# Kernel optimization log

Hardware: AMD Instinct MI355X
Metric: run time of the kernel (lower is better)

Reference implementation:

```python
import jax, jax.numpy as jnp
import numpy as np

B = 32768
K = 8           # moe_num_experts
LATENT = 256    # latent_dim
COND = 1024     # fusion_hidden_dim
HID = 128       # moe_expert_hidden_dim
EIN = LATENT + COND + 1  # expert input dim = 1281


def setup_inputs() -> dict:
    key = jax.random.key(0)
    ks = jax.random.split(key, 12)
    cond = jax.random.normal(ks[0], (B, COND), dtype=jnp.float32)
    u = jax.random.normal(ks[1], (B, LATENT), dtype=jnp.float32)
    tau = jax.random.uniform(ks[2], (B, 1), dtype=jnp.float32)
    # posterior gate: positive, sums to 1 over K (realistic p_hat)
    p_raw = jax.random.uniform(ks[3], (B, K), dtype=jnp.float32)
    p_hat = p_raw / jnp.sum(p_raw, axis=-1, keepdims=True)
    s = 0.02
    W1 = jax.random.normal(ks[4], (K, EIN, HID), dtype=jnp.float32) * s
    b1 = jnp.zeros((K, HID), dtype=jnp.float32)
    W2 = jax.random.normal(ks[5], (K, HID, HID), dtype=jnp.float32) * s
    b2 = jnp.zeros((K, HID), dtype=jnp.float32)
    W3 = jax.random.normal(ks[6], (K, HID, LATENT), dtype=jnp.float32) * s
    b3 = jnp.zeros((K, LATENT), dtype=jnp.float32)
    return {"cond": cond, "u": u, "tau": tau, "p_hat": p_hat,
            "W1": W1, "b1": b1, "W2": W2, "b2": b2, "W3": W3, "b3": b3}


def reference(cond, u, tau, p_hat, W1, b1, W2, b2, W3, b3):
    # Training path: gate = p_hat (no smooth switching, no running gate).
    x = jnp.concatenate([u, cond, tau], axis=-1)           # (B, EIN)
    h = jax.nn.silu(jnp.einsum('bd,kdh->bkh', x, W1) + b1) # (B, K, HID)
    h = jax.nn.silu(jnp.einsum('bkh,khg->bkg', h, W2) + b2)
    v_experts = jnp.einsum('bkg,kgl->bkl', h, W3) + b3     # (B, K, LATENT)
    v = jnp.einsum('bk,bkl->bl', p_hat, v_experts)         # (B, LATENT)
    return v
```

## Files before the change

kernel.cpp:

```cpp
#include <hip/hip_runtime.h>
#include <stdint.h>

typedef unsigned short u16;
typedef __attribute__((ext_vector_type(8))) short short8;
typedef __attribute__((ext_vector_type(4))) float f32x4;
typedef __attribute__((ext_vector_type(4))) uint32_t u32x4;

#define KEXP   8
#define LATENT 256
#define CONDD  1024
#define HID    128
#define EIN    1281
#define EINP   1344
#define NCH    21
#define NTOT   1024
#define BROWS  32768

__device__ __forceinline__ u16 f2bf(float x) {
  uint32_t v = __float_as_uint(x);
  v += 0x7fffu + ((v >> 16) & 1u);
  return (u16)(v >> 16);
}

__device__ __forceinline__ void async16(const void* g, void* l) {
  __builtin_amdgcn_global_load_lds(
      (const __attribute__((address_space(1))) void*)g,
      (__attribute__((address_space(3))) void*)l, 16, 0, 0);
}

__device__ __forceinline__ float silu(float x) { return x / (1.f + __expf(-x)); }

#define W1_TILES (KEXP * 42 * 4)
#define W2_TILES (KEXP * 4 * 4)
#define W3_TILES (KEXP * 4 * 8)

__global__ void conv_w(const float* __restrict__ W1, const float* __restrict__ W2,
                       const float* __restrict__ W3,
                       u16* __restrict__ W1t, u16* __restrict__ W2t, u16* __restrict__ W3t2) {
  __shared__ float t[32][33];
  const int bid = blockIdx.x;
  const int tx = threadIdx.x & 31, ty = threadIdx.x >> 5;
  if (bid < W1_TILES) {
    int k = bid / 168, r = bid % 168;
    int d0 = (r / 4) * 32, h0 = (r % 4) * 32;
    const float* src = W1 + (size_t)k * EIN * HID;
    #pragma unroll
    for (int s = 0; s < 4; ++s) {
      int d = d0 + ty + s * 8;
      t[ty + s * 8][tx] = (d < EIN) ? src[(size_t)d * HID + h0 + tx] : 0.f;
    }
    __syncthreads();
    u16* dst = W1t + (size_t)k * HID * EINP;
    #pragma unroll
    for (int s = 0; s < 4; ++s)
      dst[(size_t)(h0 + ty + s * 8) * EINP + d0 + tx] = f2bf(t[tx][ty + s * 8]);
  } else if (bid < W1_TILES + W2_TILES) {
    int j = bid - W1_TILES;
    int k = j / 16, r = j % 16;
    int d0 = (r / 4) * 32, h0 = (r % 4) * 32;
    const float* src = W2 + (size_t)k * HID * HID;
    #pragma unroll
    for (int s = 0; s < 4; ++s)
      t[ty + s * 8][tx] = src[(size_t)(d0 + ty + s * 8) * HID + h0 + tx];
    __syncthreads();
    u16* dst = W2t + (size_t)k * HID * HID;
    #pragma unroll
    for (int s = 0; s < 4; ++s)
      dst[(size_t)(h0 + ty + s * 8) * HID + d0 + tx] = f2bf(t[tx][ty + s * 8]);
  } else {
    int j = bid - W1_TILES - W2_TILES;
    int k = j / 32, r = j % 32;
    int d0 = (r / 8) * 32, h0 = (r % 8) * 32;
    const float* src = W3 + (size_t)k * HID * LATENT;
    #pragma unroll
    for (int s = 0; s < 4; ++s)
      t[ty + s * 8][tx] = src[(size_t)(d0 + ty + s * 8) * LATENT + h0 + tx];
    __syncthreads();
    #pragma unroll
    for (int s = 0; s < 4; ++s)
      W3t2[(size_t)(h0 + ty + s * 8) * NTOT + k * HID + d0 + tx] = f2bf(t[tx][ty + s * 8]);
  }
}

#define XGRP (BROWS * 168)

__global__ __launch_bounds__(256)
void x_conv(const float* __restrict__ cond, const float* __restrict__ uu,
            const float* __restrict__ tau, u16* __restrict__ Xbf) {
  int g = blockIdx.x * 256 + threadIdx.x;
  if (g >= XGRP) return;
  int row = g / 168;
  int c8  = g - row * 168;
  float f0 = 0.f, f1 = 0.f, f2 = 0.f, f3 = 0.f, f4 = 0.f, f5 = 0.f, f6 = 0.f, f7 = 0.f;
  if (c8 < 32) {
    const float4* p = (const float4*)(uu + (size_t)row * LATENT + c8 * 8);
    float4 a = p[0], b = p[1];
    f0 = a.x; f1 = a.y; f2 = a.z; f3 = a.w; f4 = b.x; f5 = b.y; f6 = b.z; f7 = b.w;
  } else if (c8 < 160) {
    const float4* p = (const float4*)(cond + (size_t)row * CONDD + (c8 - 32) * 8);
    float4 a = p[0], b = p[1];
    f0 = a.x; f1 = a.y; f2 = a.z; f3 = a.w; f4 = b.x; f5 = b.y; f6 = b.z; f7 = b.w;
  } else if (c8 == 160) {
    f0 = tau[row];
  }
  u32x4 pk;
  pk[0] = (uint32_t)f2bf(f0) | ((uint32_t)f2bf(f1) << 16);
  pk[1] = (uint32_t)f2bf(f2) | ((uint32_t)f2bf(f3) << 16);
  pk[2] = (uint32_t)f2bf(f4) | ((uint32_t)f2bf(f5) << 16);
  pk[3] = (uint32_t)f2bf(f6) | ((uint32_t)f2bf(f7) << 16);
  *(u32x4*)(Xbf + (size_t)row * EINP + c8 * 8) = pk;
}

__global__ __launch_bounds__(256, 2)
void h1_fused(const u16* __restrict__ Xbf, const u16* __restrict__ W1t,
              const float* __restrict__ b1, const u16* __restrict__ W2t,
              const float* __restrict__ b2, const float* __restrict__ p_hat,
              u16* __restrict__ H) {
  __shared__ struct {
    union {
      struct { u16 As[2][128 * 64]; u16 Bs[2][128 * 64]; } s;
      struct { u16 As2[128 * 128]; u16 Bs2[2][128 * 64]; } g;
      u16 Cs[128 * 72];
    } u;
    float Ps[128];
  } sm;

  const int tid  = threadIdx.x;
  const int wave = tid >> 6;
  const int lane = tid & 63;
  const int q    = lane >> 4;
  const int ln   = lane & 15;
  const int wm   = wave >> 1, wn = wave & 1;
  const int bid  = blockIdx.x;
  const int mt   = ((bid >> 6) << 3) | (bid & 7);
  const int e    = (bid >> 3) & 7;
  const int m0   = mt * 128;
  const u16* w1k = W1t + (size_t)e * HID * EINP;
  const u16* xtb = Xbf + (size_t)m0 * EINP;

  if (tid < 128) sm.Ps[tid] = p_hat[(size_t)(m0 + tid) * KEXP + e];

  const f32x4 fz = {0.f, 0.f, 0.f, 0.f};
  f32x4 acc[4][4];
  #pragma unroll
  for (int m = 0; m < 4; ++m)
    #pragma unroll
    for (int n = 0; n < 4; ++n) acc[m][n] = fz;

  const int rloc = lane >> 3;
  const int gsw  = lane & 7;
  const int gsrc = gsw ^ rloc;

  #pragma unroll
  for (int i = 0; i < 4; ++i) {
    int rbase = (wave * 4 + i) * 8;
    async16(xtb + (size_t)(rbase + rloc) * EINP + gsrc * 8, &sm.u.s.As[0][rbase * 64]);
    async16(w1k + (size_t)(rbase + rloc) * EINP + gsrc * 8, &sm.u.s.Bs[0][rbase * 64]);
  }

  #pragma unroll 1
  for (int ic = 0; ic < NCH; ++ic) {
    const int bf = ic & 1;
    if (ic + 1 < NCH) {
      const int d0 = (ic + 1) * 64;
      #pragma unroll
      for (int i = 0; i < 4; ++i) {
        int rbase = (wave * 4 + i) * 8;
        async16(xtb + (size_t)(rbase + rloc) * EINP + d0 + gsrc * 8,
                &sm.u.s.As[bf ^ 1][rbase * 64]);
        async16(w1k + (size_t)(rbase + rloc) * EINP + d0 + gsrc * 8,
                &sm.u.s.Bs[bf ^ 1][rbase * 64]);
      }
      asm volatile("s_waitcnt vmcnt(8)" ::: "memory");
    } else {
      asm volatile("s_waitcnt vmcnt(0)" ::: "memory");
    }
    __builtin_amdgcn_s_barrier();
    __builtin_amdgcn_sched_barrier(0);

    const u16* Ab = sm.u.s.As[bf];
    const u16* Bb = sm.u.s.Bs[bf];
    __builtin_amdgcn_s_setprio(1);
    #pragma unroll
    for (int ks = 0; ks < 2; ++ks) {
      short8 a[4], b[4];
      #pragma unroll
      for (int m = 0; m < 4; ++m) {
        int r = wm * 64 + m * 16 + ln;
        int g = (ks * 4 + q) ^ (r & 7);
        a[m] = *(const short8*)(&Ab[r * 64 + g * 8]);
      }
      #pragma unroll
      for (int n = 0; n < 4; ++n) {
        int c = wn * 64 + n * 16 + ln;
        int g = (ks * 4 + q) ^ (c & 7);
        b[n] = *(const short8*)(&Bb[c * 64 + g * 8]);
      }
      #pragma unroll
      for (int m = 0; m < 4; ++m)
        #pragma unroll
        for (int n = 0; n < 4; ++n)
          acc[m][n] = __builtin_amdgcn_mfma_f32_16x16x32_bf16(a[m], b[n], acc[m][n], 0, 0, 0);
    }
    __builtin_amdgcn_s_setprio(0);
    __builtin_amdgcn_sched_barrier(0);
    __builtin_amdgcn_s_barrier();
  }
  __syncthreads();

  const u16* w2k = W2t + (size_t)e * HID * HID;
  #pragma unroll
  for (int kc = 0; kc < 2; ++kc)
    #pragma unroll
    for (int i = 0; i < 4; ++i) {
      int rbase = (wave * 4 + i) * 8;
      async16(w2k + (size_t)(rbase + rloc) * HID + kc * 64 + gsrc * 8,
              &sm.u.g.Bs2[kc][rbase * 64]);
    }

  #pragma unroll
  for (int n = 0; n < 4; ++n) {
    int cl = wn * 64 + n * 16 + ln;
    float bv = b1[e * HID + cl];
    #pragma unroll
    for (int m = 0; m < 4; ++m)
      #pragma unroll
      for (int r = 0; r < 4; ++r) {
        int row = wm * 64 + m * 16 + q * 4 + r;
        sm.u.g.As2[row * 128 + (((cl >> 3) ^ (row & 7)) << 3) + (cl & 7)] =
            f2bf(silu(acc[m][n][r] + bv));
      }
  }

  f32x4 acc2[4][4];
  #pragma unroll
  for (int m = 0; m < 4; ++m)
    #pragma unroll
    for (int n = 0; n < 4; ++n) acc2[m][n] = fz;

  __syncthreads();

  #pragma unroll
  for (int kc = 0; kc < 2; ++kc) {
    #pragma unroll
    for (int ks = 0; ks < 2; ++ks) {
      short8 a[4], b[4];
      #pragma unroll
      for (int m = 0; m < 4; ++m) {
        int r = wm * 64 + m * 16 + ln;
        int G = kc * 8 + ks * 4 + q;
        int g = (G & 8) | ((G ^ (r & 7)) & 7);
        a[m] = *(const short8*)(&sm.u.g.As2[r * 128 + g * 8]);
      }
      #pragma unroll
      for (int n = 0; n < 4; ++n) {
        int c = wn * 64 + n * 16 + ln;
        int g = (ks * 4 + q) ^ (c & 7);
        b[n] = *(const short8*)(&sm.u.g.Bs2[kc][c * 64 + g * 8]);
      }
      #pragma unroll
      for (int m = 0; m < 4; ++m)
        #pragma unroll
        for (int n = 0; n < 4; ++n)
          acc2[m][n] = __builtin_amdgcn_mfma_f32_16x16x32_bf16(a[m], b[n], acc2[m][n], 0, 0, 0);
    }
  }
  __syncthreads();

  u16* hb = H + (size_t)m0 * NTOT + e * HID;
  #pragma unroll 1
  for (int hf = 0; hf < 2; ++hf) {
    if (wn == hf) {
      #pragma unroll
      for (int n = 0; n < 4; ++n) {
        int cl = n * 16 + ln;
        float bv = b2[e * HID + hf * 64 + cl];
        #pragma unroll
        for (int m = 0; m < 4; ++m)
          #pragma unroll
          for (int r = 0; r < 4; ++r) {
            int row = wm * 64 + m * 16 + q * 4 + r;
            sm.u.Cs[row * 72 + cl] = f2bf(sm.Ps[row] * silu(acc2[m][n][r] + bv));
          }
      }
    }
    __syncthreads();
    #pragma unroll
    for (int i = 0; i < 4; ++i) {
      int lin = tid + i * 256;
      int row = lin >> 3;
      int grp = lin & 7;
      *(u32x4*)(hb + (size_t)row * NTOT + hf * 64 + grp * 8) =
          *(const u32x4*)(&sm.u.Cs[row * 72 + grp * 8]);
    }
    __syncthreads();
  }
}

__global__ __launch_bounds__(256, 4)
void h1_gemm(const float* __restrict__ cond, const float* __restrict__ uu,
             const float* __restrict__ tau, const u16* __restrict__ W1t,
             const float* __restrict__ b1, u16* __restrict__ H1) {
  __shared__ union {
    struct { u16 As[128 * 64]; u16 Bs[128 * 64]; } s;
    u16 Cs[128 * 72];
  } sm;

  const int tid  = threadIdx.x;
  const int wave = tid >> 6;
  const int lane = tid & 63;
  const int q    = lane >> 4;
  const int ln   = lane & 15;
  const int wm   = wave >> 1, wn = wave & 1;
  const int bid  = blockIdx.x;
  const int mt   = ((bid >> 6) << 3) | (bid & 7);
  const int e    = (bid >> 3) & 7;
  const int m0   = mt * 128, n0 = e * 128;
  const u16* w1k = W1t + (size_t)e * HID * EINP;

  const f32x4 fz = {0.f, 0.f, 0.f, 0.f};
  f32x4 acc[4][4];
  #pragma unroll
  for (int m = 0; m < 4; ++m)
    #pragma unroll
    for (int n = 0; n < 4; ++n) acc[m][n] = fz;

  #pragma unroll 1
  for (int ic = 0; ic < NCH; ++ic) {
    const int d0 = ic * 64;
    #pragma unroll
    for (int i = 0; i < 4; ++i) {
      int lin  = tid + i * 256;
      int row  = lin >> 3;
      int gsw  = lin & 7;
      int gsrc = gsw ^ (row & 7);
      int gr   = m0 + row;
      float f0, f1, f2, f3, f4, f5, f6, f7;
      if (d0 < 256) {
        const float4* p = (const float4*)(uu + (size_t)gr * LATENT + d0 + gsrc * 8);
        float4 A = p[0], Bv = p[1];
        f0 = A.x; f1 = A.y; f2 = A.z; f3 = A.w; f4 = Bv.x; f5 = Bv.y; f6 = Bv.z; f7 = Bv.w;
      } else if (d0 < 1280) {
        const float4* p = (const float4*)(cond + (size_t)gr * CONDD + (d0 - 256) + gsrc * 8);
        float4 A = p[0], Bv = p[1];
        f0 = A.x; f1 = A.y; f2 = A.z; f3 = A.w; f4 = Bv.x; f5 = Bv.y; f6 = Bv.z; f7 = Bv.w;
      } else {
        float tv = tau[gr];
        f0 = (gsrc == 0) ? tv : 0.f;
        f1 = f2 = f3 = f4 = f5 = f6 = f7 = 0.f;
      }
      u32x4 pk;
      pk[0] = (uint32_t)f2bf(f0) | ((uint32_t)f2bf(f1) << 16);
      pk[1] = (uint32_t)f2bf(f2) | ((uint32_t)f2bf(f3) << 16);
      pk[2] = (uint32_t)f2bf(f4) | ((uint32_t)f2bf(f5) << 16);
      pk[3] = (uint32_t)f2bf(f6) | ((uint32_t)f2bf(f7) << 16);
      *(u32x4*)(&sm.s.As[row * 64 + gsw * 8]) = pk;
    }
    {
      int rloc = lane >> 3;
      int gsw  = lane & 7;
      int gsrc = gsw ^ rloc;
      #pragma unroll
      for (int i = 0; i < 4; ++i) {
        int rbase = (wave * 4 + i) * 8;
        async16(w1k + (size_t)(rbase + rloc) * EINP + d0 + gsrc * 8,
                &sm.s.Bs[rbase * 64]);
      }
    }
    __syncthreads();
    #pragma unroll
    for (int ks = 0; ks < 2; ++ks) {
      short8 a[4], b[4];
      #pragma unroll
      for (int m = 0; m < 4; ++m) {
        int r = wm * 64 + m * 16 + ln;
        int g = (ks * 4 + q) ^ (r & 7);
        a[m] = *(const short8*)(&sm.s.As[r * 64 + g * 8]);
      }
      #pragma unroll
      for (int n = 0; n < 4; ++n) {
        int c = wn * 64 + n * 16 + ln;
        int g = (ks * 4 + q) ^ (c & 7);
        b[n] = *(const short8*)(&sm.s.Bs[c * 64 + g * 8]);
      }
      #pragma unroll
      for (int m = 0; m < 4; ++m)
        #pragma unroll
        for (int n = 0; n < 4; ++n)
          acc[m][n] = __builtin_amdgcn_mfma_f32_16x16x32_bf16(a[m], b[n], acc[m][n], 0, 0, 0);
    }
    __syncthreads();
  }

  #pragma unroll 1
  for (int hf = 0; hf < 2; ++hf) {
    if (wn == hf) {
      #pragma unroll
      for (int n = 0; n < 4; ++n) {
        int cl = n * 16 + ln;
        float bv = b1[n0 + hf * 64 + cl];
        #pragma unroll
        for (int m = 0; m < 4; ++m)
          #pragma unroll
          for (int r = 0; r < 4; ++r)
            sm.Cs[(wm * 64 + m * 16 + q * 4 + r) * 72 + cl] = f2bf(silu(acc[m][n][r] + bv));
      }
    }
    __syncthreads();
    #pragma unroll
    for (int i = 0; i < 4; ++i) {
      int lin = tid + i * 256;
      int row = lin >> 3;
      int grp = lin & 7;
      *(u32x4*)(H1 + (size_t)(m0 + row) * NTOT + n0 + hf * 64 + grp * 8) =
          *(const u32x4*)(&sm.Cs[row * 72 + grp * 8]);
    }
    __syncthreads();
  }
}

__global__ __launch_bounds__(256, 4)
void h2_gemm(u16* __restrict__ H, const float* __restrict__ p_hat,
             const u16* __restrict__ W2t, const float* __restrict__ b2) {
  __shared__ struct {
    union { struct { u16 As[128 * 64]; u16 Bs[128 * 64]; } s; u16 Cs[128 * 72]; } u;
    float Ps[128];
  } sm;

  const int tid  = threadIdx.x;
  const int wave = tid >> 6;
  const int lane = tid & 63;
  const int q    = lane >> 4;
  const int ln   = lane & 15;
  const int wm   = wave >> 1, wn = wave & 1;
  const int mt   = blockIdx.x >> 3;
  const int e    = blockIdx.x & 7;
  const int row0 = mt * 128;

  if (tid < 128) sm.Ps[tid] = p_hat[(size_t)(row0 + tid) * KEXP + e];

  const u16* w2k = W2t + (size_t)e * HID * HID;
  u16* hb = H + (size_t)row0 * NTOT + e * HID;

  const f32x4 fz = {0.f, 0.f, 0.f, 0.f};
  f32x4 acc[4][4];
  #pragma unroll
  for (int m = 0; m < 4; ++m)
    #pragma unroll
    for (int n = 0; n < 4; ++n) acc[m][n] = fz;

  const int rloc = lane >> 3;
  const int gsw  = lane & 7;
  const int gsrc = gsw ^ rloc;

  #pragma unroll 1
  for (int kc = 0; kc < 2; ++kc) {
    #pragma unroll
    for (int i = 0; i < 4; ++i) {
      int rbase = (wave * 4 + i) * 8;
      async16(hb + (size_t)(rbase + rloc) * NTOT + kc * 64 + gsrc * 8,
              &sm.u.s.As[rbase * 64]);
      async16(w2k + (size_t)(rbase + rloc) * HID + kc * 64 + gsrc * 8,
              &sm.u.s.Bs[rbase * 64]);
    }
    __syncthreads();
    #pragma unroll
    for (int ks = 0; ks < 2; ++ks) {
      short8 a[4], b[4];
      #pragma unroll
      for (int m = 0; m < 4; ++m) {
        int r = wm * 64 + m * 16 + ln;
        int g = (ks * 4 + q) ^ (r & 7);
        a[m] = *(const short8*)(&sm.u.s.As[r * 64 + g * 8]);
      }
      #pragma unroll
      for (int n = 0; n < 4; ++n) {
        int c = wn * 64 + n * 16 + ln;
        int g = (ks * 4 + q) ^ (c & 7);
        b[n] = *(const short8*)(&sm.u.s.Bs[c * 64 + g * 8]);
      }
      #pragma unroll
      for (int m = 0; m < 4; ++m)
        #pragma unroll
        for (int n = 0; n < 4; ++n)
          acc[m][n] = __builtin_amdgcn_mfma_f32_16x16x32_bf16(a[m], b[n], acc[m][n], 0, 0, 0);
    }
    __syncthreads();
  }

  #pragma unroll 1
  for (int hf = 0; hf < 2; ++hf) {
    if (wn == hf) {
      #pragma unroll
      for (int n = 0; n < 4; ++n) {
        int cl = n * 16 + ln;
        float bv = b2[e * HID + hf * 64 + cl];
        #pragma unroll
        for (int m = 0; m < 4; ++m)
          #pragma unroll
          for (int r = 0; r < 4; ++r) {
            int row = wm * 64 + m * 16 + q * 4 + r;
            sm.u.Cs[row * 72 + cl] = f2bf(sm.Ps[row] * silu(acc[m][n][r] + bv));
          }
      }
    }
    __syncthreads();
    #pragma unroll
    for (int i = 0; i < 4; ++i) {
      int lin = tid + i * 256;
      int row = lin >> 3;
      int grp = lin & 7;
      *(u32x4*)(hb + (size_t)row * NTOT + hf * 64 + grp * 8) =
          *(const u32x4*)(&sm.u.Cs[row * 72 + grp * 8]);
    }
    __syncthreads();
  }
}

__global__ __launch_bounds__(256, 2)
void out_gemm(const u16* __restrict__ H, const float* __restrict__ p_hat,
              const u16* __restrict__ W3t2, const float* __restrict__ b3,
              float* __restrict__ out) {
  __shared__ struct {
    u16 As[2][64 * 64];
    u16 Bs[2][128 * 64];
    float Ps[64 * 8];
    float B3s[128 * 8];
  } sm;

  const int tid  = threadIdx.x;
  const int wave = tid >> 6;
  const int lane = tid & 63;
  const int q    = lane >> 4;
  const int ln   = lane & 15;
  const int bid  = blockIdx.x;
  const int mt   = ((bid >> 4) << 3) | (bid & 7);
  const int bn   = (bid >> 3) & 1;
  const int m0   = mt * 64, n0 = bn * 128;

  if (tid < 128) {
    int row = tid >> 1, h = tid & 1;
    *(float4*)(&sm.Ps[row * 8 + h * 4]) = *(const float4*)(p_hat + (size_t)(m0 + row) * KEXP + h * 4);
  }
  #pragma unroll
  for (int i = 0; i < 4; ++i) {
    int k = i * 2 + (tid >> 7);
    int c = tid & 127;
    sm.B3s[c * 8 + k] = b3[k * LATENT + n0 + c];
  }

  const f32x4 fz = {0.f, 0.f, 0.f, 0.f};
  f32x4 acc[4][2];
  #pragma unroll
  for (int m = 0; m < 4; ++m) { acc[m][0] = fz; acc[m][1] = fz; }

  const int rloc = lane >> 3;
  const int gsw  = lane & 7;
  const int gsrc = gsw ^ rloc;

  #pragma unroll
  for (int i = 0; i < 2; ++i) {
    int rbase = (wave * 2 + i) * 8;
    async16(H + (size_t)(m0 + rbase + rloc) * NTOT + gsrc * 8, &sm.As[0][rbase * 64]);
  }
  #pragma unroll
  for (int i = 0; i < 4; ++i) {
    int rbase = (wave * 4 + i) * 8;
    async16(W3t2 + (size_t)(n0 + rbase + rloc) * NTOT + gsrc * 8, &sm.Bs[0][rbase * 64]);
  }

  #pragma unroll 1
  for (int kc = 0; kc < 16; ++kc) {
    const int bf = kc & 1;
    if (kc + 1 < 16) {
      const int d0 = (kc + 1) * 64;
      #pragma unroll
      for (int i = 0; i < 2; ++i) {
        int rbase = (wave * 2 + i) * 8;
        async16(H + (size_t)(m0 + rbase + rloc) * NTOT + d0 + gsrc * 8,
                &sm.As[bf ^ 1][rbase * 64]);
      }
      #pragma unroll
      for (int i = 0; i < 4; ++i) {
        int rbase = (wave * 4 + i) * 8;
        async16(W3t2 + (size_t)(n0 + rbase + rloc) * NTOT + d0 + gsrc * 8,
                &sm.Bs[bf ^ 1][rbase * 64]);
      }
      asm volatile("s_waitcnt vmcnt(6)" ::: "memory");
    } else {
      asm volatile("s_waitcnt vmcnt(0)" ::: "memory");
    }
    __builtin_amdgcn_s_barrier();
    __builtin_amdgcn_sched_barrier(0);

    const u16* Ab = sm.As[bf];
    const u16* Bb = sm.Bs[bf];
    __builtin_amdgcn_s_setprio(1);
    #pragma unroll
    for (int ks = 0; ks < 2; ++ks) {
      short8 a[4], b[2];
      #pragma unroll
      for (int m = 0; m < 4; ++m) {
        int r = m * 16 + ln;
        int g = (ks * 4 + q) ^ (r & 7);
        a[m] = *(const short8*)(&Ab[r * 64 + g * 8]);
      }
      #pragma unroll
      for (int n = 0; n < 2; ++n) {
        int c = wave * 32 + n * 16 + ln;
        int g = (ks * 4 + q) ^ (c & 7);
        b[n] = *(const short8*)(&Bb[c * 64 + g * 8]);
      }
      #pragma unroll
      for (int m = 0; m < 4; ++m)
        #pragma unroll
        for (int n = 0; n < 2; ++n)
          acc[m][n] = __builtin_amdgcn_mfma_f32_16x16x32_bf16(a[m], b[n], acc[m][n], 0, 0, 0);
    }
    __builtin_amdgcn_s_setprio(0);
    __builtin_amdgcn_sched_barrier(0);
    __builtin_amdgcn_s_barrier();
  }
  __syncthreads();

  #pragma unroll
  for (int n = 0; n < 2; ++n) {
    int col = wave * 32 + n * 16 + ln;
    float4 c0 = *(const float4*)(&sm.B3s[col * 8]);
    float4 c1 = *(const float4*)(&sm.B3s[col * 8 + 4]);
    #pragma unroll
    for (int m = 0; m < 4; ++m)
      #pragma unroll
      for (int r = 0; r < 4; ++r) {
        int row = m * 16 + q * 4 + r;
        float4 p0 = *(const float4*)(&sm.Ps[row * 8]);
        float4 p1 = *(const float4*)(&sm.Ps[row * 8 + 4]);
        float v = acc[m][n][r]
                + p0.x * c0.x + p0.y * c0.y + p0.z * c0.z + p0.w * c0.w
                + p1.x * c1.x + p1.y * c1.y + p1.z * c1.z + p1.w * c1.w;
        out[(size_t)(m0 + row) * LATENT + n0 + col] = v;
      }
  }
}

extern "C" void kernel_launch(void* const* d_in, const int* in_sizes, int n_in,
                              void* d_out, int out_size, void* d_ws, size_t ws_size,
                              hipStream_t stream) {
  const float* cond  = (const float*)d_in[0];
  const float* u     = (const float*)d_in[1];
  const float* tau   = (const float*)d_in[2];
  const float* p_hat = (const float*)d_in[3];
  const float* W1    = (const float*)d_in[4];
  const float* b1    = (const float*)d_in[5];
  const float* W2    = (const float*)d_in[6];
  const float* b2    = (const float*)d_in[7];
  const float* W3    = (const float*)d_in[8];
  const float* b3    = (const float*)d_in[9];
  float* out = (float*)d_out;

  const size_t N1 = (size_t)KEXP * HID * EINP;
  const size_t N2 = (size_t)KEXP * HID * HID;
  const size_t N3 = (size_t)LATENT * NTOT;
  const size_t NH = (size_t)BROWS * NTOT;
  const size_t NX = (size_t)BROWS * EINP;

  u16* W1t  = (u16*)d_ws;
  u16* W2t  = W1t + N1;
  u16* W3t2 = W2t + N2;
  u16* H    = W3t2 + N3;

  if (ws_size >= (N1 + N2 + N3 + NH + NX) * sizeof(u16)) {
    u16* Xbf = H + NH;
    conv_w<<<W1_TILES + W2_TILES + W3_TILES, 256, 0, stream>>>(W1, W2, W3, W1t, W2t, W3t2);
    x_conv<<<XGRP / 256, 256, 0, stream>>>(cond, u, tau, Xbf);
    h1_fused<<<2048, 256, 0, stream>>>(Xbf, W1t, b1, W2t, b2, p_hat, H);
    out_gemm<<<1024, 256, 0, stream>>>(H, p_hat, W3t2, b3, out);
  } else if (ws_size >= (N1 + N2 + N3 + NH) * sizeof(u16)) {
    conv_w<<<W1_TILES + W2_TILES + W3_TILES, 256, 0, stream>>>(W1, W2, W3, W1t, W2t, W3t2);
    h1_gemm<<<2048, 256, 0, stream>>>(cond, u, tau, W1t, b1, H);
    h2_gemm<<<2048, 256, 0, stream>>>(H, p_hat, W2t, b2);
    out_gemm<<<1024, 256, 0, stream>>>(H, p_hat, W3t2, b3, out);
  }
}
```

Measured before the change: 435.7 us.

## Merge weight and input conversion kernels; restructure GEMM K-loops as unrolled double-buffer

```diff
diff --git a/kernel.cpp b/kernel.cpp
--- a/kernel.cpp
+++ b/kernel.cpp
@@ -33,12 +33,42 @@
 #define W1_TILES (KEXP * 42 * 4)
 #define W2_TILES (KEXP * 4 * 4)
 #define W3_TILES (KEXP * 4 * 8)
-
-__global__ void conv_w(const float* __restrict__ W1, const float* __restrict__ W2,
-                       const float* __restrict__ W3,
-                       u16* __restrict__ W1t, u16* __restrict__ W2t, u16* __restrict__ W3t2) {
+#define WCONV_TILES (W1_TILES + W2_TILES + W3_TILES)
+#define XGRP (BROWS * 168)
+#define XBLK (XGRP / 256)
+
+__global__ __launch_bounds__(256)
+void prep(const float* __restrict__ W1, const float* __restrict__ W2,
+          const float* __restrict__ W3, const float* __restrict__ cond,
+          const float* __restrict__ uu, const float* __restrict__ tau,
+          u16* __restrict__ W1t, u16* __restrict__ W2t, u16* __restrict__ W3t2,
+          u16* __restrict__ Xbf) {
   __shared__ float t[32][33];
   const int bid = blockIdx.x;
+  if (bid >= WCONV_TILES) {
+    int g = (bid - WCONV_TILES) * 256 + threadIdx.x;
+    int row = g / 168;
+    int c8  = g - row * 168;
+    float f0 = 0.f, f1 = 0.f, f2 = 0.f, f3 = 0.f, f4 = 0.f, f5 = 0.f, f6 = 0.f, f7 = 0.f;
+    if (c8 < 32) {
+      const float4* p = (const float4*)(uu + (size_t)row * LATENT + c8 * 8);
+      float4 a = p[0], b = p[1];
+      f0 = a.x; f1 = a.y; f2 = a.z; f3 = a.w; f4 = b.x; f5 = b.y; f6 = b.z; f7 = b.w;
+    } else if (c8 < 160) {
+      const float4* p = (const float4*)(cond + (size_t)row * CONDD + (c8 - 32) * 8);
+      float4 a = p[0], b = p[1];
+      f0 = a.x; f1 = a.y; f2 = a.z; f3 = a.w; f4 = b.x; f5 = b.y; f6 = b.z; f7 = b.w;
+    } else if (c8 == 160) {
+      f0 = tau[row];
+    }
+    u32x4 pk;
+    pk[0] = (uint32_t)f2bf(f0) | ((uint32_t)f2bf(f1) << 16);
+    pk[1] = (uint32_t)f2bf(f2) | ((uint32_t)f2bf(f3) << 16);
+    pk[2] = (uint32_t)f2bf(f4) | ((uint32_t)f2bf(f5) << 16);
+    pk[3] = (uint32_t)f2bf(f6) | ((uint32_t)f2bf(f7) << 16);
+    *(u32x4*)(Xbf + (size_t)row * EINP + c8 * 8) = pk;
+    return;
+  }
   const int tx = threadIdx.x & 31, ty = threadIdx.x >> 5;
   if (bid < W1_TILES) {
     int k = bid / 168, r = bid % 168;
@@ -80,35 +110,6 @@
     for (int s = 0; s < 4; ++s)
       W3t2[(size_t)(h0 + ty + s * 8) * NTOT + k * HID + d0 + tx] = f2bf(t[tx][ty + s * 8]);
   }
-}
-
-#define XGRP (BROWS * 168)
-
-__global__ __launch_bounds__(256)
-void x_conv(const float* __restrict__ cond, const float* __restrict__ uu,
-            const float* __restrict__ tau, u16* __restrict__ Xbf) {
-  int g = blockIdx.x * 256 + threadIdx.x;
-  if (g >= XGRP) return;
-  int row = g / 168;
-  int c8  = g - row * 168;
-  float f0 = 0.f, f1 = 0.f, f2 = 0.f, f3 = 0.f, f4 = 0.f, f5 = 0.f, f6 = 0.f, f7 = 0.f;
-  if (c8 < 32) {
-    const float4* p = (const float4*)(uu + (size_t)row * LATENT + c8 * 8);
-    float4 a = p[0], b = p[1];
-    f0 = a.x; f1 = a.y; f2 = a.z; f3 = a.w; f4 = b.x; f5 = b.y; f6 = b.z; f7 = b.w;
-  } else if (c8 < 160) {
-    const float4* p = (const float4*)(cond + (size_t)row * CONDD + (c8 - 32) * 8);
-    float4 a = p[0], b = p[1];
-    f0 = a.x; f1 = a.y; f2 = a.z; f3 = a.w; f4 = b.x; f5 = b.y; f6 = b.z; f7 = b.w;
-  } else if (c8 == 160) {
-    f0 = tau[row];
-  }
-  u32x4 pk;
-  pk[0] = (uint32_t)f2bf(f0) | ((uint32_t)f2bf(f1) << 16);
-  pk[1] = (uint32_t)f2bf(f2) | ((uint32_t)f2bf(f3) << 16);
-  pk[2] = (uint32_t)f2bf(f4) | ((uint32_t)f2bf(f5) << 16);
-  pk[3] = (uint32_t)f2bf(f6) | ((uint32_t)f2bf(f7) << 16);
-  *(u32x4*)(Xbf + (size_t)row * EINP + c8 * 8) = pk;
 }
 
 __global__ __launch_bounds__(256, 2)
@@ -151,33 +152,17 @@
   const int gsw  = lane & 7;
   const int gsrc = gsw ^ rloc;
 
-  #pragma unroll
-  for (int i = 0; i < 4; ++i) {
-    int rbase = (wave * 4 + i) * 8;
-    async16(xtb + (size_t)(rbase + rloc) * EINP + gsrc * 8, &sm.u.s.As[0][rbase * 64]);
-    async16(w1k + (size_t)(rbase + rloc) * EINP + gsrc * 8, &sm.u.s.Bs[0][rbase * 64]);
-  }
-
-  #pragma unroll 1
-  for (int ic = 0; ic < NCH; ++ic) {
-    const int bf = ic & 1;
-    if (ic + 1 < NCH) {
-      const int d0 = (ic + 1) * 64;
-      #pragma unroll
-      for (int i = 0; i < 4; ++i) {
-        int rbase = (wave * 4 + i) * 8;
-        async16(xtb + (size_t)(rbase + rloc) * EINP + d0 + gsrc * 8,
-                &sm.u.s.As[bf ^ 1][rbase * 64]);
-        async16(w1k + (size_t)(rbase + rloc) * EINP + d0 + gsrc * 8,
-                &sm.u.s.Bs[bf ^ 1][rbase * 64]);
-      }
-      asm volatile("s_waitcnt vmcnt(8)" ::: "memory");
-    } else {
-      asm volatile("s_waitcnt vmcnt(0)" ::: "memory");
-    }
-    __builtin_amdgcn_s_barrier();
-    __builtin_amdgcn_sched_barrier(0);
-
+  auto stage = [&](int d0, int bf) {
+    #pragma unroll
+    for (int i = 0; i < 4; ++i) {
+      int rbase = (wave * 4 + i) * 8;
+      async16(xtb + (size_t)(rbase + rloc) * EINP + d0 + gsrc * 8,
+              &sm.u.s.As[bf][rbase * 64]);
+      async16(w1k + (size_t)(rbase + rloc) * EINP + d0 + gsrc * 8,
+              &sm.u.s.Bs[bf][rbase * 64]);
+    }
+  };
+  auto mfma_chunk = [&](int bf) {
     const u16* Ab = sm.u.s.As[bf];
     const u16* Bb = sm.u.s.Bs[bf];
     __builtin_amdgcn_s_setprio(1);
@@ -203,9 +188,28 @@
           acc[m][n] = __builtin_amdgcn_mfma_f32_16x16x32_bf16(a[m], b[n], acc[m][n], 0, 0, 0);
     }
     __builtin_amdgcn_s_setprio(0);
+  };
+
+  stage(0, 0);
+  asm volatile("s_waitcnt vmcnt(0)" ::: "memory");
+  __builtin_amdgcn_s_barrier();
+  __builtin_amdgcn_sched_barrier(0);
+
+  #pragma unroll 1
+  for (int ic2 = 0; ic2 < 10; ++ic2) {
+    const int d = ic2 * 128;
+    stage(d + 64, 1);
+    mfma_chunk(0);
+    asm volatile("s_waitcnt vmcnt(0)" ::: "memory");
+    __builtin_amdgcn_s_barrier();
     __builtin_amdgcn_sched_barrier(0);
+    stage(d + 128, 0);
+    mfma_chunk(1);
+    asm volatile("s_waitcnt vmcnt(0)" ::: "memory");
     __builtin_amdgcn_s_barrier();
-  }
+    __builtin_amdgcn_sched_barrier(0);
+  }
+  mfma_chunk(0);
   __syncthreads();
 
   const u16* w2k = W2t + (size_t)e * HID * HID;
@@ -294,6 +298,132 @@
           *(const u32x4*)(&sm.u.Cs[row * 72 + grp * 8]);
     }
     __syncthreads();
+  }
+}
+
+__global__ __launch_bounds__(256, 2)
+void out_gemm(const u16* __restrict__ H, const float* __restrict__ p_hat,
+              const u16* __restrict__ W3t2, const float* __restrict__ b3,
+              float* __restrict__ out) {
+  __shared__ struct {
+    u16 As[2][64 * 64];
+    u16 Bs[2][128 * 64];
+    float Ps[64 * 8];
+    float B3s[128 * 8];
+  } sm;
+
+  const int tid  = threadIdx.x;
+  const int wave = tid >> 6;
+  const int lane = tid & 63;
+  const int q    = lane >> 4;
+  const int ln   = lane & 15;
+  const int bid  = blockIdx.x;
+  const int mt   = ((bid >> 4) << 3) | (bid & 7);
+  const int bn   = (bid >> 3) & 1;
+  const int m0   = mt * 64, n0 = bn * 128;
+
+  if (tid < 128) {
+    int row = tid >> 1, h = tid & 1;
+    *(float4*)(&sm.Ps[row * 8 + h * 4]) = *(const float4*)(p_hat + (size_t)(m0 + row) * KEXP + h * 4);
+  }
+  #pragma unroll
+  for (int i = 0; i < 4; ++i) {
+    int k = i * 2 + (tid >> 7);
+    int c = tid & 127;
+    sm.B3s[c * 8 + k] = b3[k * LATENT + n0 + c];
+  }
+
+  const f32x4 fz = {0.f, 0.f, 0.f, 0.f};
+  f32x4 acc[4][2];
+  #pragma unroll
+  for (int m = 0; m < 4; ++m) { acc[m][0] = fz; acc[m][1] = fz; }
+
+  const int rloc = lane >> 3;
+  const int gsw  = lane & 7;
+  const int gsrc = gsw ^ rloc;
+
+  auto stage = [&](int d0, int bf) {
+    #pragma unroll
+    for (int i = 0; i < 2; ++i) {
+      int rbase = (wave * 2 + i) * 8;
+      async16(H + (size_t)(m0 + rbase + rloc) * NTOT + d0 + gsrc * 8,
+              &sm.As[bf][rbase * 64]);
+    }
+    #pragma unroll
+    for (int i = 0; i < 4; ++i) {
+      int rbase = (wave * 4 + i) * 8;
+      async16(W3t2 + (size_t)(n0 + rbase + rloc) * NTOT + d0 + gsrc * 8,
+              &sm.Bs[bf][rbase * 64]);
+    }
+  };
+  auto mfma_chunk = [&](int bf) {
+    const u16* Ab = sm.As[bf];
+    const u16* Bb = sm.Bs[bf];
+    __builtin_amdgcn_s_setprio(1);
+    #pragma unroll
+    for (int ks = 0; ks < 2; ++ks) {
+      short8 a[4], b[2];
+      #pragma unroll
+      for (int m = 0; m < 4; ++m) {
+        int r = m * 16 + ln;
+        int g = (ks * 4 + q) ^ (r & 7);
+        a[m] = *(const short8*)(&Ab[r * 64 + g * 8]);
+      }
+      #pragma unroll
+      for (int n = 0; n < 2; ++n) {
+        int c = wave * 32 + n * 16 + ln;
+        int g = (ks * 4 + q) ^ (c & 7);
+        b[n] = *(const short8*)(&Bb[c * 64 + g * 8]);
+      }
+      #pragma unroll
+      for (int m = 0; m < 4; ++m)
+        #pragma unroll
+        for (int n = 0; n < 2; ++n)
+          acc[m][n] = __builtin_amdgcn_mfma_f32_16x16x32_bf16(a[m], b[n], acc[m][n], 0, 0, 0);
+    }
+    __builtin_amdgcn_s_setprio(0);
+  };
+
+  stage(0, 0);
+  asm volatile("s_waitcnt vmcnt(0)" ::: "memory");
+  __builtin_amdgcn_s_barrier();
+  __builtin_amdgcn_sched_barrier(0);
+
+  #pragma unroll 1
+  for (int k2 = 0; k2 < 8; ++k2) {
+    const int d = k2 * 128;
+    stage(d + 64, 1);
+    mfma_chunk(0);
+    asm volatile("s_waitcnt vmcnt(0)" ::: "memory");
+    __builtin_amdgcn_s_barrier();
+    __builtin_amdgcn_sched_barrier(0);
+    if (k2 < 7) {
+      stage(d + 128, 0);
+      mfma_chunk(1);
+      asm volatile("s_waitcnt vmcnt(0)" ::: "memory");
+      __builtin_amdgcn_s_barrier();
+      __builtin_amdgcn_sched_barrier(0);
+    }
+  }
+  mfma_chunk(1);
+
+  #pragma unroll
+  for (int n = 0; n < 2; ++n) {
+    int col = wave * 32 + n * 16 + ln;
+    float4 c0 = *(const float4*)(&sm.B3s[col * 8]);
+    float4 c1 = *(const float4*)(&sm.B3s[col * 8 + 4]);
+    #pragma unroll
+    for (int m = 0; m < 4; ++m)
+      #pragma unroll
+      for (int r = 0; r < 4; ++r) {
+        int row = m * 16 + q * 4 + r;
+        float4 p0 = *(const float4*)(&sm.Ps[row * 8]);
+        float4 p1 = *(const float4*)(&sm.Ps[row * 8 + 4]);
+        float v = acc[m][n][r]
+                + p0.x * c0.x + p0.y * c0.y + p0.z * c0.z + p0.w * c0.w
+                + p1.x * c1.x + p1.y * c1.y + p1.z * c1.z + p1.w * c1.w;
+        out[(size_t)(m0 + row) * LATENT + n0 + col] = v;
+      }
   }
 }
 
@@ -517,132 +647,6 @@
   }
 }
 
-__global__ __launch_bounds__(256, 2)
-void out_gemm(const u16* __restrict__ H, const float* __restrict__ p_hat,
-              const u16* __restrict__ W3t2, const float* __restrict__ b3,
-              float* __restrict__ out) {
-  __shared__ struct {
-    u16 As[2][64 * 64];
-    u16 Bs[2][128 * 64];
-    float Ps[64 * 8];
-    float B3s[128 * 8];
-  } sm;
-
-  const int tid  = threadIdx.x;
-  const int wave = tid >> 6;
-  const int lane = tid & 63;
-  const int q    = lane >> 4;
-  const int ln   = lane & 15;
-  const int bid  = blockIdx.x;
-  const int mt   = ((bid >> 4) << 3) | (bid & 7);
-  const int bn   = (bid >> 3) & 1;
-  const int m0   = mt * 64, n0 = bn * 128;
-
-  if (tid < 128) {
-    int row = tid >> 1, h = tid & 1;
-    *(float4*)(&sm.Ps[row * 8 + h * 4]) = *(const float4*)(p_hat + (size_t)(m0 + row) * KEXP + h * 4);
-  }
-  #pragma unroll
-  for (int i = 0; i < 4; ++i) {
-    int k = i * 2 + (tid >> 7);
-    int c = tid & 127;
-    sm.B3s[c * 8 + k] = b3[k * LATENT + n0 + c];
-  }
-
-  const f32x4 fz = {0.f, 0.f, 0.f, 0.f};
-  f32x4 acc[4][2];
-  #pragma unroll
-  for (int m = 0; m < 4; ++m) { acc[m][0] = fz; acc[m][1] = fz; }
-
-  const int rloc = lane >> 3;
-  const int gsw  = lane & 7;
-  const int gsrc = gsw ^ rloc;
-
-  #pragma unroll
-  for (int i = 0; i < 2; ++i) {
-    int rbase = (wave * 2 + i) * 8;
-    async16(H + (size_t)(m0 + rbase + rloc) * NTOT + gsrc * 8, &sm.As[0][rbase * 64]);
-  }
-  #pragma unroll
-  for (int i = 0; i < 4; ++i) {
-    int rbase = (wave * 4 + i) * 8;
-    async16(W3t2 + (size_t)(n0 + rbase + rloc) * NTOT + gsrc * 8, &sm.Bs[0][rbase * 64]);
-  }
-
-  #pragma unroll 1
-  for (int kc = 0; kc < 16; ++kc) {
-    const int bf = kc & 1;
-    if (kc + 1 < 16) {
-      const int d0 = (kc + 1) * 64;
-      #pragma unroll
-      for (int i = 0; i < 2; ++i) {
-        int rbase = (wave * 2 + i) * 8;
-        async16(H + (size_t)(m0 + rbase + rloc) * NTOT + d0 + gsrc * 8,
-                &sm.As[bf ^ 1][rbase * 64]);
-      }
-      #pragma unroll
-      for (int i = 0; i < 4; ++i) {
-        int rbase = (wave * 4 + i) * 8;
-        async16(W3t2 + (size_t)(n0 + rbase + rloc) * NTOT + d0 + gsrc * 8,
-                &sm.Bs[bf ^ 1][rbase * 64]);
-      }
-      asm volatile("s_waitcnt vmcnt(6)" ::: "memory");
-    } else {
-      asm volatile("s_waitcnt vmcnt(0)" ::: "memory");
-    }
-    __builtin_amdgcn_s_barrier();
-    __builtin_amdgcn_sched_barrier(0);
-
-    const u16* Ab = sm.As[bf];
-    const u16* Bb = sm.Bs[bf];
-    __builtin_amdgcn_s_setprio(1);
-    #pragma unroll
-    for (int ks = 0; ks < 2; ++ks) {
-      short8 a[4], b[2];
-      #pragma unroll
-      for (int m = 0; m < 4; ++m) {
-        int r = m * 16 + ln;
-        int g = (ks * 4 + q) ^ (r & 7);
-        a[m] = *(const short8*)(&Ab[r * 64 + g * 8]);
-      }
-      #pragma unroll
-      for (int n = 0; n < 2; ++n) {
-        int c = wave * 32 + n * 16 + ln;
-        int g = (ks * 4 + q) ^ (c & 7);
-        b[n] = *(const short8*)(&Bb[c * 64 + g * 8]);
-      }
-      #pragma unroll
-      for (int m = 0; m < 4; ++m)
-        #pragma unroll
-        for (int n = 0; n < 2; ++n)
-          acc[m][n] = __builtin_amdgcn_mfma_f32_16x16x32_bf16(a[m], b[n], acc[m][n], 0, 0, 0);
-    }
-    __builtin_amdgcn_s_setprio(0);
-    __builtin_amdgcn_sched_barrier(0);
-    __builtin_amdgcn_s_barrier();
-  }
-  __syncthreads();
-
-  #pragma unroll
-  for (int n = 0; n < 2; ++n) {
-    int col = wave * 32 + n * 16 + ln;
-    float4 c0 = *(const float4*)(&sm.B3s[col * 8]);
-    float4 c1 = *(const float4*)(&sm.B3s[col * 8 + 4]);
-    #pragma unroll
-    for (int m = 0; m < 4; ++m)
-      #pragma unroll
-      for (int r = 0; r < 4; ++r) {
-        int row = m * 16 + q * 4 + r;
-        float4 p0 = *(const float4*)(&sm.Ps[row * 8]);
-        float4 p1 = *(const float4*)(&sm.Ps[row * 8 + 4]);
-        float v = acc[m][n][r]
-                + p0.x * c0.x + p0.y * c0.y + p0.z * c0.z + p0.w * c0.w
-                + p1.x * c1.x + p1.y * c1.y + p1.z * c1.z + p1.w * c1.w;
-        out[(size_t)(m0 + row) * LATENT + n0 + col] = v;
-      }
-  }
-}
-
 extern "C" void kernel_launch(void* const* d_in, const int* in_sizes, int n_in,
                               void* d_out, int out_size, void* d_ws, size_t ws_size,
                               hipStream_t stream) {
@@ -671,12 +675,13 @@
 
   if (ws_size >= (N1 + N2 + N3 + NH + NX) * sizeof(u16)) {
     u16* Xbf = H + NH;
-    conv_w<<<W1_TILES + W2_TILES + W3_TILES, 256, 0, stream>>>(W1, W2, W3, W1t, W2t, W3t2);
-    x_conv<<<XGRP / 256, 256, 0, stream>>>(cond, u, tau, Xbf);
+    prep<<<WCONV_TILES + XBLK, 256, 0, stream>>>(W1, W2, W3, cond, u, tau,
+                                                 W1t, W2t, W3t2, Xbf);
     h1_fused<<<2048, 256, 0, stream>>>(Xbf, W1t, b1, W2t, b2, p_hat, H);
     out_gemm<<<1024, 256, 0, stream>>>(H, p_hat, W3t2, b3, out);
   } else if (ws_size >= (N1 + N2 + N3 + NH) * sizeof(u16)) {
-    conv_w<<<W1_TILES + W2_TILES + W3_TILES, 256, 0, stream>>>(W1, W2, W3, W1t, W2t, W3t2);
+    prep<<<WCONV_TILES, 256, 0, stream>>>(W1, W2, W3, cond, u, tau,
+                                          W1t, W2t, W3t2, (u16*)nullptr);
     h1_gemm<<<2048, 256, 0, stream>>>(cond, u, tau, W1t, b1, H);
     h2_gemm<<<2048, 256, 0, stream>>>(H, p_hat, W2t, b2);
     out_gemm<<<1024, 256, 0, stream>>>(H, p_hat, W3t2, b3, out);
```

Measured after the change: 431.7 us. No clear change (-0.9%).
